# Performance work log

Hardware: AMD Instinct MI355X
Metric: run time of the kernel (lower is better)

## Reference

```python
import jax, jax.numpy as jnp
import numpy as np

B, C, A = 65536, 300, 32  # batch, n_cards, n_archetypes


def setup_inputs() -> dict:
    key = jax.random.key(0)
    k1, k2, k3 = jax.random.split(key, 3)
    # options: binary availability mask; ensure >=1 option per row so the
    # sign-aware log-softmax never sees an all-zero row.
    options = (jax.random.uniform(k1, (B, C)) < 0.05).astype(jnp.float32)
    options = options.at[:, 0].set(1.0)
    # cards: nonnegative held-card counts (0..2)
    cards = jax.random.randint(k2, (B, C), 0, 3).astype(jnp.float32)
    X = jnp.concatenate([options, cards], axis=1)  # (B, 2*C)
    W = jax.random.uniform(k3, (C, A), dtype=jnp.float32)  # archetype weights
    return {"X": X, "W": W}


def stable_non_zero_log_softmax(x):
    # Sign-aware stabilized log-softmax: zero entries stay exactly zero.
    s = jnp.sign(x)
    b = jnp.max(x, axis=1, keepdims=True)
    stab = x - b * s
    lse = jnp.log(jnp.sum(s * jnp.exp(stab), axis=1, keepdims=True))
    return s * (stab - lse)


def reference(X, W):
    n_cards = W.shape[0]
    options, cards = X[:, :n_cards], X[:, n_cards:]
    # archetype preferences per pick: (B, A)
    ap = cards @ W + 1.0
    # einsum('pw,pcw->pc', ap, options[:,:,None]*W[None]) == options * (ap @ W.T)
    scores = options * (ap @ W.T)  # (B, C)
    return stable_non_zero_log_softmax(scores)
```

## Files before the change

kernel.cpp:

```cpp
#include <hip/hip_runtime.h>
#include <math.h>

typedef _Float16 half8 __attribute__((ext_vector_type(8)));
typedef float f32x4 __attribute__((ext_vector_type(4)));

namespace {
constexpr int kB = 65536;
constexpr int kC = 300;
constexpr int kA = 32;
constexpr int kBlock = 512;
constexpr int kRowsPerBlock = 128;
constexpr int kWTS = 328;
constexpr int kWrS = 40;
constexpr int kApS = 40;
}

template <int kCtrl>
__device__ __forceinline__ float dpp_rot(float x) {
    int yi = __builtin_amdgcn_update_dpp(0, __builtin_bit_cast(int, x), kCtrl, 0xf, 0xf, false);
    return __builtin_bit_cast(float, yi);
}
__device__ __forceinline__ float rsum16(float x) {
    x += dpp_rot<0x128>(x);
    x += dpp_rot<0x124>(x);
    x += dpp_rot<0x122>(x);
    x += dpp_rot<0x121>(x);
    return x;
}
__device__ __forceinline__ float rmax16(float x) {
    x = fmaxf(x, dpp_rot<0x128>(x));
    x = fmaxf(x, dpp_rot<0x124>(x));
    x = fmaxf(x, dpp_rot<0x122>(x));
    x = fmaxf(x, dpp_rot<0x121>(x));
    return x;
}

__global__ __launch_bounds__(kBlock) void draftbot_kernel(
    const float* __restrict__ X,
    const float* __restrict__ W,
    float* __restrict__ out)
{
    __shared__ _Float16 WT[kA * kWTS];
    __shared__ _Float16 Wr[304 * kWrS];
    __shared__ _Float16 ap_s[8][16 * kApS];

    const int tid  = threadIdx.x;
    const int lane = tid & 63;
    const int wid  = tid >> 6;
    const int lm = lane & 15;
    const int lq = lane >> 4;
    const int ko = lq * 8;
    const size_t r0 = (size_t)blockIdx.x * kRowsPerBlock + wid * 16;

    unsigned int obit[4];
    #pragma unroll
    for (int j = 0; j < 4; ++j) {
        const float* __restrict__ ox = X + (r0 + 4 * lq + j) * (size_t)(2 * kC);
        unsigned int b = 0;
        #pragma unroll
        for (int n = 0; n < 19; ++n) {
            const int c = 16 * n + lm;
            if (c < kC && ox[c] != 0.0f) b |= (1u << n);
        }
        obit[j] = b;
    }

    for (int e = tid; e < kC * kA; e += kBlock) {
        const int c = e >> 5;
        const int a = e & 31;
        const _Float16 h = (_Float16)W[e];
        WT[a * kWTS + c] = h;
        Wr[c * kWrS + a] = h;
    }
    for (int e = tid; e < kA * (kWTS - kC); e += kBlock) {
        const int a = e / (kWTS - kC);
        const int c = kC + e % (kWTS - kC);
        WT[a * kWTS + c] = (_Float16)0.0f;
    }
    if (tid < 4 * kWrS) Wr[kC * kWrS + tid] = (_Float16)0.0f;
    __syncthreads();

    const float* __restrict__ crow = X + (r0 + lm) * (size_t)(2 * kC) + kC;
    f32x4 acc0 = {0.f, 0.f, 0.f, 0.f};
    f32x4 acc1 = {0.f, 0.f, 0.f, 0.f};
    #pragma unroll
    for (int s = 0; s < 9; ++s) {
        const float4 u = *reinterpret_cast<const float4*>(crow + 32 * s + ko);
        const float4 v = *reinterpret_cast<const float4*>(crow + 32 * s + ko + 4);
        const half8 Af = { (_Float16)u.x, (_Float16)u.y, (_Float16)u.z, (_Float16)u.w,
                           (_Float16)v.x, (_Float16)v.y, (_Float16)v.z, (_Float16)v.w };
        const half8 B0 = *reinterpret_cast<const half8*>(&WT[lm * kWTS + 32 * s + ko]);
        const half8 B1 = *reinterpret_cast<const half8*>(&WT[(16 + lm) * kWTS + 32 * s + ko]);
        acc0 = __builtin_amdgcn_mfma_f32_16x16x32_f16(Af, B0, acc0, 0, 0, 0);
        acc1 = __builtin_amdgcn_mfma_f32_16x16x32_f16(Af, B1, acc1, 0, 0, 0);
    }
    {
        float av[8];
        #pragma unroll
        for (int j = 0; j < 8; ++j) {
            const int k = 288 + ko + j;
            av[j] = (k < kC) ? crow[k] : 0.0f;
        }
        const half8 Af = { (_Float16)av[0], (_Float16)av[1], (_Float16)av[2], (_Float16)av[3],
                           (_Float16)av[4], (_Float16)av[5], (_Float16)av[6], (_Float16)av[7] };
        const half8 B0 = *reinterpret_cast<const half8*>(&WT[lm * kWTS + 288 + ko]);
        const half8 B1 = *reinterpret_cast<const half8*>(&WT[(16 + lm) * kWTS + 288 + ko]);
        acc0 = __builtin_amdgcn_mfma_f32_16x16x32_f16(Af, B0, acc0, 0, 0, 0);
        acc1 = __builtin_amdgcn_mfma_f32_16x16x32_f16(Af, B1, acc1, 0, 0, 0);
    }

    _Float16* __restrict__ aps = ap_s[wid];
    #pragma unroll
    for (int j = 0; j < 4; ++j) {
        const int rr = 4 * lq + j;
        aps[rr * kApS + lm]      = (_Float16)(acc0[j] + 1.0f);
        aps[rr * kApS + 16 + lm] = (_Float16)(acc1[j] + 1.0f);
    }
    asm volatile("s_waitcnt lgkmcnt(0)" ::: "memory");
    __builtin_amdgcn_sched_barrier(0);
    const half8 A2 = *reinterpret_cast<const half8*>(&aps[lm * kApS + ko]);

    const f32x4 zz = {0.f, 0.f, 0.f, 0.f};

    f32x4 mj = {0.f, 0.f, 0.f, 0.f};
    #pragma unroll
    for (int n = 0; n < 19; ++n) {
        const half8 Bn = *reinterpret_cast<const half8*>(&Wr[(16 * n + lm) * kWrS + ko]);
        const f32x4 c4 = __builtin_amdgcn_mfma_f32_16x16x32_f16(A2, Bn, zz, 0, 0, 0);
        #pragma unroll
        for (int j = 0; j < 4; ++j) {
            const float x = ((obit[j] >> n) & 1u) ? c4[j] : 0.0f;
            mj[j] = fmaxf(mj[j], x);
        }
    }
    #pragma unroll
    for (int j = 0; j < 4; ++j) mj[j] = rmax16(mj[j]);

    f32x4 Sj = {0.f, 0.f, 0.f, 0.f};
    #pragma unroll
    for (int n = 0; n < 19; ++n) {
        const half8 Bn = *reinterpret_cast<const half8*>(&Wr[(16 * n + lm) * kWrS + ko]);
        const f32x4 c4 = __builtin_amdgcn_mfma_f32_16x16x32_f16(A2, Bn, zz, 0, 0, 0);
        #pragma unroll
        for (int j = 0; j < 4; ++j) {
            const float x = ((obit[j] >> n) & 1u) ? c4[j] : 0.0f;
            const float sg = (x > 0.f ? 1.f : 0.f) - (x < 0.f ? 1.f : 0.f);
            Sj[j] += sg * __expf(fmaf(-mj[j], sg, x));
        }
    }
    f32x4 lse;
    #pragma unroll
    for (int j = 0; j < 4; ++j) lse[j] = __logf(rsum16(Sj[j]));

    #pragma unroll
    for (int n = 0; n < 19; ++n) {
        const half8 Bn = *reinterpret_cast<const half8*>(&Wr[(16 * n + lm) * kWrS + ko]);
        const f32x4 c4 = __builtin_amdgcn_mfma_f32_16x16x32_f16(A2, Bn, zz, 0, 0, 0);
        const int c = 16 * n + lm;
        if (c < kC) {
            #pragma unroll
            for (int j = 0; j < 4; ++j) {
                const float x = ((obit[j] >> n) & 1u) ? c4[j] : 0.0f;
                const float sg = (x > 0.f ? 1.f : 0.f) - (x < 0.f ? 1.f : 0.f);
                out[(r0 + 4 * lq + j) * (size_t)kC + c] = sg * (fmaf(-mj[j], sg, x) - lse[j]);
            }
        }
    }
}

extern "C" void kernel_launch(void* const* d_in, const int* in_sizes, int n_in,
                              void* d_out, int out_size, void* d_ws, size_t ws_size,
                              hipStream_t stream) {
    const float* X = (const float*)d_in[0];
    const float* W = (const float*)d_in[1];
    float* out = (float*)d_out;
    dim3 grid(kB / kRowsPerBlock);
    dim3 block(kBlock);
    hipLaunchKernelGGL(draftbot_kernel, grid, block, 0, stream, X, W, out);
}
```

Baseline: 56.47 us.

## Split fused kernel into two launches staging archetype preferences in workspace

Splits the single fused kernel into two kernels. The first computes ap = cards@W+1 and writes it as fp16 to the workspace buffer. The second reloads ap, rebuilds the option bitmask and the W tile, and runs the score GEMM with the sign-aware log-softmax. Each kernel uses less shared memory and fewer registers, which may raise occupancy. The cost is an extra launch, a global round trip for ap, and rebuilding the W tile in both kernels.

New measurement: 53.81 us. -4.7%, faster.

```diff
diff --git a/kernel.cpp b/kernel.cpp
--- a/kernel.cpp
+++ b/kernel.cpp
@@ -12,7 +12,6 @@
 constexpr int kRowsPerBlock = 128;
 constexpr int kWTS = 328;
 constexpr int kWrS = 40;
-constexpr int kApS = 40;
 }
 
 template <int kCtrl>
@@ -35,14 +34,12 @@
     return x;
 }
 
-__global__ __launch_bounds__(kBlock) void draftbot_kernel(
+__global__ __launch_bounds__(kBlock) void gemm1_kernel(
     const float* __restrict__ X,
     const float* __restrict__ W,
-    float* __restrict__ out)
+    _Float16* __restrict__ apws)
 {
     __shared__ _Float16 WT[kA * kWTS];
-    __shared__ _Float16 Wr[304 * kWrS];
-    __shared__ _Float16 ap_s[8][16 * kApS];
 
     const int tid  = threadIdx.x;
     const int lane = tid & 63;
@@ -52,32 +49,16 @@
     const int ko = lq * 8;
     const size_t r0 = (size_t)blockIdx.x * kRowsPerBlock + wid * 16;
 
-    unsigned int obit[4];
-    #pragma unroll
-    for (int j = 0; j < 4; ++j) {
-        const float* __restrict__ ox = X + (r0 + 4 * lq + j) * (size_t)(2 * kC);
-        unsigned int b = 0;
-        #pragma unroll
-        for (int n = 0; n < 19; ++n) {
-            const int c = 16 * n + lm;
-            if (c < kC && ox[c] != 0.0f) b |= (1u << n);
-        }
-        obit[j] = b;
-    }
-
     for (int e = tid; e < kC * kA; e += kBlock) {
         const int c = e >> 5;
         const int a = e & 31;
-        const _Float16 h = (_Float16)W[e];
-        WT[a * kWTS + c] = h;
-        Wr[c * kWrS + a] = h;
+        WT[a * kWTS + c] = (_Float16)W[e];
     }
     for (int e = tid; e < kA * (kWTS - kC); e += kBlock) {
         const int a = e / (kWTS - kC);
         const int c = kC + e % (kWTS - kC);
         WT[a * kWTS + c] = (_Float16)0.0f;
     }
-    if (tid < 4 * kWrS) Wr[kC * kWrS + tid] = (_Float16)0.0f;
     __syncthreads();
 
     const float* __restrict__ crow = X + (r0 + lm) * (size_t)(2 * kC) + kC;
@@ -109,16 +90,52 @@
         acc1 = __builtin_amdgcn_mfma_f32_16x16x32_f16(Af, B1, acc1, 0, 0, 0);
     }
 
-    _Float16* __restrict__ aps = ap_s[wid];
     #pragma unroll
     for (int j = 0; j < 4; ++j) {
-        const int rr = 4 * lq + j;
-        aps[rr * kApS + lm]      = (_Float16)(acc0[j] + 1.0f);
-        aps[rr * kApS + 16 + lm] = (_Float16)(acc1[j] + 1.0f);
+        const size_t base = (r0 + 4 * lq + j) * (size_t)kA;
+        apws[base + lm]      = (_Float16)(acc0[j] + 1.0f);
+        apws[base + 16 + lm] = (_Float16)(acc1[j] + 1.0f);
     }
-    asm volatile("s_waitcnt lgkmcnt(0)" ::: "memory");
-    __builtin_amdgcn_sched_barrier(0);
-    const half8 A2 = *reinterpret_cast<const half8*>(&aps[lm * kApS + ko]);
+}
+
+__global__ __launch_bounds__(kBlock) void gemm2_kernel(
+    const float* __restrict__ X,
+    const float* __restrict__ W,
+    const _Float16* __restrict__ apws,
+    float* __restrict__ out)
+{
+    __shared__ _Float16 Wr[304 * kWrS];
+
+    const int tid  = threadIdx.x;
+    const int lane = tid & 63;
+    const int wid  = tid >> 6;
+    const int lm = lane & 15;
+    const int lq = lane >> 4;
+    const int ko = lq * 8;
+    const size_t r0 = (size_t)blockIdx.x * kRowsPerBlock + wid * 16;
+
+    const half8 A2 = *reinterpret_cast<const half8*>(&apws[(r0 + lm) * (size_t)kA + ko]);
+
+    unsigned int obit[4];
+    #pragma unroll
+    for (int j = 0; j < 4; ++j) {
+        const float* __restrict__ ox = X + (r0 + 4 * lq + j) * (size_t)(2 * kC);
+        unsigned int b = 0;
+        #pragma unroll
+        for (int n = 0; n < 19; ++n) {
+            const int c = 16 * n + lm;
+            if (c < kC && ox[c] != 0.0f) b |= (1u << n);
+        }
+        obit[j] = b;
+    }
+
+    for (int e = tid; e < kC * kA; e += kBlock) {
+        const int c = e >> 5;
+        const int a = e & 31;
+        Wr[c * kWrS + a] = (_Float16)W[e];
+    }
+    if (tid < 4 * kWrS) Wr[kC * kWrS + tid] = (_Float16)0.0f;
+    __syncthreads();
 
     const f32x4 zz = {0.f, 0.f, 0.f, 0.f};
 
@@ -174,7 +191,9 @@
     const float* X = (const float*)d_in[0];
     const float* W = (const float*)d_in[1];
     float* out = (float*)d_out;
+    _Float16* apws = (_Float16*)d_ws;
     dim3 grid(kB / kRowsPerBlock);
     dim3 block(kBlock);
-    hipLaunchKernelGGL(draftbot_kernel, grid, block, 0, stream, X, W, out);
+    hipLaunchKernelGGL(gemm1_kernel, grid, block, 0, stream, X, W, apws);
+    hipLaunchKernelGGL(gemm2_kernel, grid, block, 0, stream, X, W, apws, out);
 }
```
